# Kernel optimization log

Hardware: AMD Instinct MI355X
Metric: run time of the kernel (lower is better)

## Reference

```python
import jax, jax.numpy as jnp
import numpy as np

B, T, D_MODEL = 2, 2048, 1024
H, D_HEAD, R = 16, 64, 16
CAUSAL = True


def setup_inputs() -> dict:
    key = jax.random.key(0)
    ks = jax.random.split(key, 6)
    return {
        "x": jax.random.normal(ks[0], (B, T, D_MODEL), dtype=jnp.float32),
        "W_qkv": jax.random.normal(ks[1], (D_MODEL, 3 * D_MODEL), dtype=jnp.float32) * 0.02,
        "W_q_lsr": jax.random.normal(ks[2], (H, D_HEAD, R), dtype=jnp.float32) * 0.1,
        "W_k_lsr": jax.random.normal(ks[3], (H, D_HEAD, R), dtype=jnp.float32) * 0.1,
        "core": jax.random.normal(ks[4], (H, R), dtype=jnp.float32),
        "W_o": jax.random.normal(ks[5], (D_MODEL, D_MODEL), dtype=jnp.float32) * 0.02,
    }


def reference(x, W_qkv, W_q_lsr, W_k_lsr, core, W_o):
    Bx, Tx, D = x.shape
    Hh, Dh, Rr = W_q_lsr.shape
    # Fused QKV projection, then split heads -> (B, H, T, D_head)
    qkv = x @ W_qkv  # (B, T, 3D)
    q, k, v = jnp.split(qkv, 3, axis=-1)
    q = q.reshape(Bx, Tx, Hh, Dh).transpose(0, 2, 1, 3)
    k = k.reshape(Bx, Tx, Hh, Dh).transpose(0, 2, 1, 3)
    v = v.reshape(Bx, Tx, Hh, Dh).transpose(0, 2, 1, 3)
    # Low-rank (LSR) projections of q and k; core + 1/sqrt(R) scaling on q side
    scale = 1.0 / jnp.sqrt(jnp.asarray(max(Rr, 1), dtype=jnp.float32))
    q_lr = jnp.einsum('bhtd,hdr->bhtr', q, W_q_lsr) * core[None, :, None, :] * scale
    k_lr = jnp.einsum('bhtd,hdr->bhtr', k, W_k_lsr)
    # Low-rank scores (B, H, T, T)
    scores = jnp.einsum('bhir,bhjr->bhij', q_lr, k_lr)
    if CAUSAL:
        mask = jnp.tril(jnp.ones((Tx, Tx), dtype=bool))
        scores = jnp.where(mask[None, None], scores, -jnp.inf)
    attn = jax.nn.softmax(scores, axis=-1)
    out = jnp.einsum('bhij,bhjd->bhid', attn, v)  # (B, H, T, D_head)
    out = out.transpose(0, 2, 1, 3).reshape(Bx, Tx, D)
    return out @ W_o
```

## Files before the change

kernel.cpp:

```cpp
#include <hip/hip_runtime.h>
#include <hip/hip_bf16.h>

#define BB 2
#define TT 2048
#define DD 1024
#define HH 16
#define DH 64
#define RR 16
#define BT (BB*TT)
#define BH (BB*HH)
#define D3 (3*DD)
#define NC 1536

typedef __bf16 bf16x8 __attribute__((ext_vector_type(8)));
typedef __bf16 bf16x4 __attribute__((ext_vector_type(4)));
typedef float f32x4 __attribute__((ext_vector_type(4)));
typedef short short4v __attribute__((ext_vector_type(4)));

__device__ __forceinline__ float bf2f(unsigned short u) {
  unsigned int v = ((unsigned int)u) << 16;
  return __builtin_bit_cast(float, v);
}
__device__ __forceinline__ unsigned short f2bf(float f) {
  unsigned int x = __builtin_bit_cast(unsigned int, f);
  unsigned int r = x + 0x7fffu + ((x >> 16) & 1u);
  return (unsigned short)(r >> 16);
}
__device__ __forceinline__ short4v pack_bf16x4(float a, float b, float c, float d) {
  uint2 u;
  u.x = (unsigned)f2bf(a) | ((unsigned)f2bf(b) << 16);
  u.y = (unsigned)f2bf(c) | ((unsigned)f2bf(d) << 16);
  return __builtin_bit_cast(short4v, u);
}
__device__ __forceinline__ short4v pack4_cvt(float a, float b, float c, float d) {
  bf16x4 v = {(__bf16)a, (__bf16)b, (__bf16)c, (__bf16)d};
  return __builtin_bit_cast(short4v, v);
}

#define NEG_BIG (-1e30f)

__device__ __forceinline__ void async_copy16(const void* g, void* l) {
  __builtin_amdgcn_global_load_lds((const __attribute__((address_space(1))) void*)g,
                                   (__attribute__((address_space(3))) void*)l, 16, 0, 0);
}

__global__ __launch_bounds__(256) void prep_fused(const float* __restrict__ x,
                                                  const float* __restrict__ Wqkv,
                                                  const float* __restrict__ Wql,
                                                  const float* __restrict__ Wkl,
                                                  const float* __restrict__ core,
                                                  const float* __restrict__ Wo,
                                                  unsigned short* __restrict__ x_bf,
                                                  unsigned short* __restrict__ Wcomb_t,
                                                  unsigned short* __restrict__ Wo_t) {
  __shared__ float tile[32][33];
  __shared__ float Aq[64][65], Ak[64][65], Lq[64][16], Lk[64][16], cs[16];
  const int bid = blockIdx.x, tid = threadIdx.x;
  if (bid < 2048) {
    int i = (bid * 256 + tid) * 8;
    float4 a = *(const float4*)&x[i];
    float4 b = *(const float4*)&x[i + 4];
    unsigned short t[8] = {f2bf(a.x), f2bf(a.y), f2bf(a.z), f2bf(a.w),
                           f2bf(b.x), f2bf(b.y), f2bf(b.z), f2bf(b.w)};
    *(uint4*)&x_bf[i] = *(const uint4*)t;
  } else if (bid < 4096) {
    const float* in; unsigned short* out; int C, coff, lb;
    if (bid < 3072) { in = Wo;   out = Wo_t;    C = DD; coff = 0;    lb = bid - 2048; }
    else            { in = Wqkv; out = Wcomb_t; C = D3; coff = 2048; lb = bid - 3072; }
    const int tx = tid & 31, ty = tid >> 5;
    const int bx = lb & 31, by = lb >> 5;
    const int xx = bx * 32 + tx, y0 = by * 32;
#pragma unroll
    for (int i = 0; i < 32; i += 8)
      tile[ty + i][tx] = in[(size_t)(y0 + ty + i) * C + coff + xx];
    __syncthreads();
    const int xo = y0 + tx, yo0 = bx * 32;
#pragma unroll
    for (int i = 0; i < 32; i += 8)
      out[(size_t)(yo0 + ty + i) * DD + xo] = f2bf(tile[tx][ty + i]);
  } else {
    const int l = bid - 4096;
    const int d0 = (l & 15) * 64, h = l >> 4;
#pragma unroll
    for (int p = 0; p < 16; p++) {
      int idx = p * 256 + tid, dd = idx >> 6, e = idx & 63;
      Aq[dd][e] = Wqkv[(size_t)(d0 + dd) * D3 + h * 64 + e];
      Ak[dd][e] = Wqkv[(size_t)(d0 + dd) * D3 + DD + h * 64 + e];
    }
#pragma unroll
    for (int p = 0; p < 4; p++) {
      int idx = p * 256 + tid, e = idx >> 4, r = idx & 15;
      Lq[e][r] = Wql[h * 1024 + e * 16 + r];
      Lk[e][r] = Wkl[h * 1024 + e * 16 + r];
    }
    if (tid < 16) cs[tid] = core[h * 16 + tid];
    __syncthreads();
    const int dd = tid & 63, rg = tid >> 6;
    float aq[4] = {}, ak[4] = {};
    for (int e = 0; e < 64; e++) {
      float xq = Aq[dd][e], xk = Ak[dd][e];
#pragma unroll
      for (int j = 0; j < 4; j++) {
        aq[j] += xq * Lq[e][rg * 4 + j];
        ak[j] += xk * Lk[e][rg * 4 + j];
      }
    }
#pragma unroll
    for (int j = 0; j < 4; j++) {
      int r = rg * 4 + j;
      Wcomb_t[(size_t)(1024 + h * 16 + r) * DD + d0 + dd] =
          f2bf(aq[j] * cs[r] * (0.25f * 1.4426950408889634f));
      Wcomb_t[(size_t)(1280 + h * 16 + r) * DD + d0 + dd] = f2bf(ak[j]);
    }
  }
}

__device__ __forceinline__ void gemm64_core(const unsigned short* __restrict__ A,
                                            const unsigned short* __restrict__ Bt,
                                            int K, int bm, int bn,
                                            int tid, int g, int c, int wm, int wn,
                                            f32x4 acc[2][4]) {
  __shared__ __attribute__((aligned(16))) unsigned short As[2][64 * 32];
  __shared__ __attribute__((aligned(16))) unsigned short Bs[2][128 * 32];
  const int e0 = tid * 8;
  const int r0 = e0 >> 5, q0 = e0 & 31;
  const unsigned short* Arow = &A[(size_t)(bm * 64 + r0) * K + q0];
  const unsigned short* Brow0 = &Bt[(size_t)(bn * 128 + r0) * K + q0];
  const unsigned short* Brow1 = &Bt[(size_t)(bn * 128 + 64 + r0) * K + q0];
  async_copy16(Arow, &As[0][e0]);
  async_copy16(Brow0, &Bs[0][e0]);
  async_copy16(Brow1, &Bs[0][2048 + e0]);
  __syncthreads();
  const int nsteps = K >> 5;
#pragma unroll 2
  for (int t = 0; t < nsteps; t++) {
    const int cur = t & 1, nxt = cur ^ 1;
    if (t + 1 < nsteps) {
      const int k1 = (t + 1) << 5;
      async_copy16(Arow + k1, &As[nxt][e0]);
      async_copy16(Brow0 + k1, &Bs[nxt][e0]);
      async_copy16(Brow1 + k1, &Bs[nxt][2048 + e0]);
    }
    bf16x8 af[2];
#pragma unroll
    for (int mt = 0; mt < 2; mt++)
      af[mt] = *(const bf16x8*)&As[cur][(wm * 32 + mt * 16 + c) * 32 + g * 8];
#pragma unroll
    for (int nt = 0; nt < 4; nt++) {
      bf16x8 bf = *(const bf16x8*)&Bs[cur][(wn * 64 + nt * 16 + c) * 32 + g * 8];
#pragma unroll
      for (int mt = 0; mt < 2; mt++)
        acc[mt][nt] = __builtin_amdgcn_mfma_f32_16x16x32_bf16(af[mt], bf, acc[mt][nt], 0, 0, 0);
    }
    __syncthreads();
  }
}

__global__ __launch_bounds__(256) void gemm64_f32(const unsigned short* __restrict__ A,
                                                  const unsigned short* __restrict__ Bt,
                                                  float* __restrict__ C,
                                                  int M, int N, int K) {
  const int tid = threadIdx.x, lane = tid & 63;
  const int g = lane >> 4, c = lane & 15;
  const int wid = tid >> 6, wm = wid >> 1, wn = wid & 1;
  const int bm = blockIdx.y, bn = blockIdx.x;
  f32x4 acc[2][4] = {};
  gemm64_core(A, Bt, K, bm, bn, tid, g, c, wm, wn, acc);
#pragma unroll
  for (int mt = 0; mt < 2; mt++)
#pragma unroll
    for (int nt = 0; nt < 4; nt++)
#pragma unroll
      for (int r = 0; r < 4; r++) {
        int row = bm * 64 + wm * 32 + mt * 16 + g * 4 + r;
        int col = bn * 128 + wn * 64 + nt * 16 + c;
        C[(size_t)row * N + col] = acc[mt][nt][r];
      }
}

__global__ __launch_bounds__(256) void gemm_fused(const unsigned short* __restrict__ A,
                                                  const unsigned short* __restrict__ Bt,
                                                  unsigned short* __restrict__ qls,
                                                  unsigned short* __restrict__ klr,
                                                  unsigned short* __restrict__ vt,
                                                  int M, int N, int K) {
  const int tid = threadIdx.x, lane = tid & 63;
  const int g = lane >> 4, c = lane & 15;
  const int wid = tid >> 6, wm = wid >> 1, wn = wid & 1;
  const int bm = blockIdx.y, bn = blockIdx.x;
  f32x4 acc[2][4] = {};
  gemm64_core(A, Bt, K, bm, bn, tid, g, c, wm, wn, acc);
#pragma unroll
  for (int mt = 0; mt < 2; mt++)
#pragma unroll
    for (int nt = 0; nt < 4; nt++) {
      int colb = bn * 128 + wn * 64 + nt * 16;
      int tg0 = bm * 64 + wm * 32 + mt * 16 + g * 4;
      int b = tg0 >> 11, t0 = tg0 & 2047;
      if (colb < 1024) {
        int h = colb >> 6, d = (colb & 63) + c;
        uint2 pk = __builtin_bit_cast(uint2, pack_bf16x4(acc[mt][nt][0], acc[mt][nt][1],
                                                         acc[mt][nt][2], acc[mt][nt][3]));
        size_t idx = (size_t)(b * 16 + h) * (TT / 4) * 256 + (size_t)(t0 >> 2) * 256 + d * 4;
        *(uint2*)&vt[idx] = pk;
      } else if (colb < 1280) {
        int h = (colb - 1024) >> 4;
        size_t base = (size_t)(b * 16 + h) * TT;
#pragma unroll
        for (int r = 0; r < 4; r++)
          qls[(base + t0 + r) * 16 + c] = f2bf(acc[mt][nt][r]);
      } else {
        int h = (colb - 1280) >> 4;
        size_t base = (size_t)(b * 16 + h) * TT;
#pragma unroll
        for (int r = 0; r < 4; r++)
          klr[(base + t0 + r) * 16 + c] = f2bf(acc[mt][nt][r]);
      }
    }
}

__global__ __launch_bounds__(256, 3) void flash_lsr(const unsigned short* __restrict__ qls,
                                                    const unsigned short* __restrict__ klr,
                                                    const unsigned short* __restrict__ vt,
                                                    unsigned short* __restrict__ attn) {
  const int bh = blockIdx.x & 31, b = bh >> 4, h = bh & 15;
  const int qt = 31 - (blockIdx.x >> 5);
  const int tid = threadIdx.x, lane = tid & 63, w = tid >> 6;
  const int g = lane >> 4, c = lane & 15;
  const int q0 = qt * 64, jmax = qt >> 1;

  __shared__ __attribute__((aligned(16))) unsigned short Ks[2][128 * 20];
  __shared__ __attribute__((aligned(16))) unsigned short Vs[2][32 * 264];

  const size_t qbase = (size_t)bh * TT;
  const short4v qf = __builtin_bit_cast(short4v,
      *(const uint2*)&qls[(qbase + q0 + w * 16 + c) * 16 + g * 4]);
  const int qg = q0 + w * 16 + c;
  float mi = NEG_BIG, li = 0.f;
  f32x4 oa[4] = {};
  const f32x4 zero = {0.f, 0.f, 0.f, 0.f};
  const size_t kb = (size_t)bh * TT * 16;
  const size_t vb = (size_t)bh * TT * 64;

  uint4 kr = *(const uint4*)&klr[kb + tid * 8];
  uint4 vr[4];
#pragma unroll
  for (int p = 0; p < 4; p++)
    vr[p] = *(const uint4*)&vt[vb + (p * 256 + tid) * 8];

  int p = 0;
  f32x4 s[8];
  for (int jt = 0; jt <= jmax; jt++) {
    *(uint4*)&Ks[p][(tid >> 1) * 20 + (tid & 1) * 8] = kr;
#pragma unroll
    for (int q = 0; q < 4; q++) {
      int e = (q * 256 + tid) * 8;
      *(uint4*)&Vs[p][(e >> 8) * 264 + (e & 255)] = vr[q];
    }
    __syncthreads();
    if (jt < jmax) {
      kr = *(const uint4*)&klr[kb + (size_t)(jt + 1) * 2048 + tid * 8];
      const unsigned short* vp = &vt[vb + (size_t)(jt + 1) * 8192];
#pragma unroll
      for (int q = 0; q < 4; q++)
        vr[q] = *(const uint4*)&vp[(q * 256 + tid) * 8];
    }
    const unsigned short* Kb = Ks[p];
#pragma unroll
    for (int nt = 0; nt < 8; nt++) {
      short4v kf = __builtin_bit_cast(short4v, *(const uint2*)&Kb[(nt * 16 + c) * 20 + g * 4]);
      s[nt] = __builtin_amdgcn_mfma_f32_16x16x16bf16_1k(kf, qf, zero, 0, 0, 0);
    }
    if (jt == jmax) {
#pragma unroll
      for (int nt = 0; nt < 8; nt++)
#pragma unroll
        for (int r = 0; r < 4; r++) {
          int jg = jt * 128 + nt * 16 + g * 4 + r;
          if (jg > qg) s[nt][r] = NEG_BIG;
        }
    }
    f32x4 vm = s[0];
#pragma unroll
    for (int nt = 1; nt < 8; nt++)
#pragma unroll
      for (int r = 0; r < 4; r++) vm[r] = fmaxf(vm[r], s[nt][r]);
    float rm = fmaxf(fmaxf(vm[0], vm[1]), fmaxf(vm[2], vm[3]));
    rm = fmaxf(rm, __shfl_xor(rm, 16, 64));
    rm = fmaxf(rm, __shfl_xor(rm, 32, 64));
    float mnew = fmaxf(mi, rm);
    float alpha = __builtin_amdgcn_exp2f(mi - mnew);
    mi = mnew;
    f32x4 vs = zero;
#pragma unroll
    for (int nt = 0; nt < 8; nt++)
#pragma unroll
      for (int r = 0; r < 4; r++) {
        float pv = __builtin_amdgcn_exp2f(s[nt][r] - mnew);
        s[nt][r] = pv;
        vs[r] += pv;
      }
    float rs = (vs[0] + vs[1]) + (vs[2] + vs[3]);
    rs += __shfl_xor(rs, 16, 64);
    rs += __shfl_xor(rs, 32, 64);
    li = li * alpha + rs;
#pragma unroll
    for (int nd = 0; nd < 4; nd++)
#pragma unroll
      for (int r = 0; r < 4; r++) oa[nd][r] *= alpha;
    const unsigned short* Vb = Vs[p];
#pragma unroll
    for (int kc = 0; kc < 8; kc++) {
      short4v pf = pack4_cvt(s[kc][0], s[kc][1], s[kc][2], s[kc][3]);
#pragma unroll
      for (int nd = 0; nd < 4; nd++) {
        uint2 vv = *(const uint2*)&Vb[(kc * 4 + g) * 264 + (nd * 16 + c) * 4];
        short4v vf = __builtin_bit_cast(short4v, vv);
        oa[nd] = __builtin_amdgcn_mfma_f32_16x16x16bf16_1k(vf, pf, oa[nd], 0, 0, 0);
      }
    }
    p ^= 1;
  }

  const float inv = 1.f / li;
  const size_t rowb = ((size_t)b * TT + q0 + w * 16 + c) * DD + h * 64;
#pragma unroll
  for (int nd = 0; nd < 4; nd++) {
    short4v pk = pack4_cvt(oa[nd][0] * inv, oa[nd][1] * inv,
                           oa[nd][2] * inv, oa[nd][3] * inv);
    *(uint2*)&attn[rowb + nd * 16 + g * 4] = __builtin_bit_cast(uint2, pk);
  }
}

extern "C" void kernel_launch(void* const* d_in, const int* in_sizes, int n_in,
                              void* d_out, int out_size, void* d_ws, size_t ws_size,
                              hipStream_t stream) {
  const float* x      = (const float*)d_in[0];
  const float* W_qkv  = (const float*)d_in[1];
  const float* W_qlsr = (const float*)d_in[2];
  const float* W_klsr = (const float*)d_in[3];
  const float* core   = (const float*)d_in[4];
  const float* W_o    = (const float*)d_in[5];
  float* out = (float*)d_out;

  char* ws = (char*)d_ws;
  unsigned short* x_bf    = (unsigned short*)ws; ws += (size_t)BT * DD * 2;
  unsigned short* Wcomb_t = (unsigned short*)ws; ws += (size_t)NC * DD * 2;
  unsigned short* Wo_t    = (unsigned short*)ws; ws += (size_t)DD * DD * 2;
  unsigned short* qls     = (unsigned short*)ws; ws += (size_t)BH * TT * 16 * 2;
  unsigned short* klr     = (unsigned short*)ws; ws += (size_t)BH * TT * 16 * 2;
  unsigned short* vt      = (unsigned short*)ws; ws += (size_t)BH * TT * 64 * 2;
  unsigned short* attn    = (unsigned short*)ws; ws += (size_t)BT * DD * 2;

  prep_fused<<<4352, 256, 0, stream>>>(x, W_qkv, W_qlsr, W_klsr, core, W_o,
                                       x_bf, Wcomb_t, Wo_t);
  gemm_fused<<<dim3(NC / 128, BT / 64), 256, 0, stream>>>(x_bf, Wcomb_t, qls, klr, vt, BT, NC, DD);
  flash_lsr<<<dim3(32 * BH), 256, 0, stream>>>(qls, klr, vt, attn);
  gemm64_f32<<<dim3(DD / 128, BT / 64), 256, 0, stream>>>(attn, Wo_t, out, BT, DD, DD);
}
```

Before: 185.9 us.

## Double GEMM K-step to 64 and read V directly from global in flash kernel

The GEMM core now stages 64-wide K slices (two 32-wide halves) per pipeline step, which halves the number of barriers and loop iterations at the cost of doubled LDS use. The flash attention kernel drops the LDS staging of V and has each wave load V fragments straight from global memory (relying on L1/L2) inside the PV MFMA loop. This removes the V LDS writes and shrinks shared memory, which could raise occupancy. The risk is exposed global-load latency on the critical MFMA path, because the V prefetch into registers is gone.

```diff
diff --git a/kernel.cpp b/kernel.cpp
--- a/kernel.cpp
+++ b/kernel.cpp
@@ -120,37 +120,45 @@
                                             int K, int bm, int bn,
                                             int tid, int g, int c, int wm, int wn,
                                             f32x4 acc[2][4]) {
-  __shared__ __attribute__((aligned(16))) unsigned short As[2][64 * 32];
-  __shared__ __attribute__((aligned(16))) unsigned short Bs[2][128 * 32];
+  __shared__ __attribute__((aligned(16))) unsigned short As[2][2 * 2048];
+  __shared__ __attribute__((aligned(16))) unsigned short Bs[2][2 * 4096];
   const int e0 = tid * 8;
   const int r0 = e0 >> 5, q0 = e0 & 31;
-  const unsigned short* Arow = &A[(size_t)(bm * 64 + r0) * K + q0];
-  const unsigned short* Brow0 = &Bt[(size_t)(bn * 128 + r0) * K + q0];
-  const unsigned short* Brow1 = &Bt[(size_t)(bn * 128 + 64 + r0) * K + q0];
-  async_copy16(Arow, &As[0][e0]);
-  async_copy16(Brow0, &Bs[0][e0]);
-  async_copy16(Brow1, &Bs[0][2048 + e0]);
+  const unsigned short* Ar  = &A[(size_t)(bm * 64 + r0) * K + q0];
+  const unsigned short* Br0 = &Bt[(size_t)(bn * 128 + r0) * K + q0];
+  const unsigned short* Br1 = &Bt[(size_t)(bn * 128 + 64 + r0) * K + q0];
+  async_copy16(Ar,       &As[0][e0]);
+  async_copy16(Ar  + 32, &As[0][2048 + e0]);
+  async_copy16(Br0,      &Bs[0][e0]);
+  async_copy16(Br1,      &Bs[0][2048 + e0]);
+  async_copy16(Br0 + 32, &Bs[0][4096 + e0]);
+  async_copy16(Br1 + 32, &Bs[0][4096 + 2048 + e0]);
   __syncthreads();
-  const int nsteps = K >> 5;
-#pragma unroll 2
+  const int nsteps = K >> 6;
   for (int t = 0; t < nsteps; t++) {
     const int cur = t & 1, nxt = cur ^ 1;
     if (t + 1 < nsteps) {
-      const int k1 = (t + 1) << 5;
-      async_copy16(Arow + k1, &As[nxt][e0]);
-      async_copy16(Brow0 + k1, &Bs[nxt][e0]);
-      async_copy16(Brow1 + k1, &Bs[nxt][2048 + e0]);
-    }
-    bf16x8 af[2];
-#pragma unroll
-    for (int mt = 0; mt < 2; mt++)
-      af[mt] = *(const bf16x8*)&As[cur][(wm * 32 + mt * 16 + c) * 32 + g * 8];
-#pragma unroll
-    for (int nt = 0; nt < 4; nt++) {
-      bf16x8 bf = *(const bf16x8*)&Bs[cur][(wn * 64 + nt * 16 + c) * 32 + g * 8];
+      const int k1 = (t + 1) << 6;
+      async_copy16(Ar  + k1,      &As[nxt][e0]);
+      async_copy16(Ar  + k1 + 32, &As[nxt][2048 + e0]);
+      async_copy16(Br0 + k1,      &Bs[nxt][e0]);
+      async_copy16(Br1 + k1,      &Bs[nxt][2048 + e0]);
+      async_copy16(Br0 + k1 + 32, &Bs[nxt][4096 + e0]);
+      async_copy16(Br1 + k1 + 32, &Bs[nxt][4096 + 2048 + e0]);
+    }
+#pragma unroll
+    for (int p = 0; p < 2; p++) {
+      bf16x8 af[2];
 #pragma unroll
       for (int mt = 0; mt < 2; mt++)
-        acc[mt][nt] = __builtin_amdgcn_mfma_f32_16x16x32_bf16(af[mt], bf, acc[mt][nt], 0, 0, 0);
+        af[mt] = *(const bf16x8*)&As[cur][p * 2048 + (wm * 32 + mt * 16 + c) * 32 + g * 8];
+#pragma unroll
+      for (int nt = 0; nt < 4; nt++) {
+        bf16x8 bf = *(const bf16x8*)&Bs[cur][p * 4096 + (wn * 64 + nt * 16 + c) * 32 + g * 8];
+#pragma unroll
+        for (int mt = 0; mt < 2; mt++)
+          acc[mt][nt] = __builtin_amdgcn_mfma_f32_16x16x32_bf16(af[mt], bf, acc[mt][nt], 0, 0, 0);
+      }
     }
     __syncthreads();
   }
@@ -230,7 +238,6 @@
   const int q0 = qt * 64, jmax = qt >> 1;
 
   __shared__ __attribute__((aligned(16))) unsigned short Ks[2][128 * 20];
-  __shared__ __attribute__((aligned(16))) unsigned short Vs[2][32 * 264];
 
   const size_t qbase = (size_t)bh * TT;
   const short4v qf = __builtin_bit_cast(short4v,
@@ -243,28 +250,14 @@
   const size_t vb = (size_t)bh * TT * 64;
 
   uint4 kr = *(const uint4*)&klr[kb + tid * 8];
-  uint4 vr[4];
-#pragma unroll
-  for (int p = 0; p < 4; p++)
-    vr[p] = *(const uint4*)&vt[vb + (p * 256 + tid) * 8];
 
   int p = 0;
   f32x4 s[8];
   for (int jt = 0; jt <= jmax; jt++) {
     *(uint4*)&Ks[p][(tid >> 1) * 20 + (tid & 1) * 8] = kr;
-#pragma unroll
-    for (int q = 0; q < 4; q++) {
-      int e = (q * 256 + tid) * 8;
-      *(uint4*)&Vs[p][(e >> 8) * 264 + (e & 255)] = vr[q];
-    }
     __syncthreads();
-    if (jt < jmax) {
+    if (jt < jmax)
       kr = *(const uint4*)&klr[kb + (size_t)(jt + 1) * 2048 + tid * 8];
-      const unsigned short* vp = &vt[vb + (size_t)(jt + 1) * 8192];
-#pragma unroll
-      for (int q = 0; q < 4; q++)
-        vr[q] = *(const uint4*)&vp[(q * 256 + tid) * 8];
-    }
     const unsigned short* Kb = Ks[p];
 #pragma unroll
     for (int nt = 0; nt < 8; nt++) {
@@ -308,13 +301,13 @@
     for (int nd = 0; nd < 4; nd++)
 #pragma unroll
       for (int r = 0; r < 4; r++) oa[nd][r] *= alpha;
-    const unsigned short* Vb = Vs[p];
+    const unsigned short* vp = &vt[vb + (size_t)jt * 8192];
 #pragma unroll
     for (int kc = 0; kc < 8; kc++) {
       short4v pf = pack4_cvt(s[kc][0], s[kc][1], s[kc][2], s[kc][3]);
 #pragma unroll
       for (int nd = 0; nd < 4; nd++) {
-        uint2 vv = *(const uint2*)&Vb[(kc * 4 + g) * 264 + (nd * 16 + c) * 4];
+        uint2 vv = *(const uint2*)&vp[(kc * 4 + g) * 256 + (nd * 16 + c) * 4];
         short4v vf = __builtin_bit_cast(short4v, vv);
         oa[nd] = __builtin_amdgcn_mfma_f32_16x16x16bf16_1k(vf, pf, oa[nd], 0, 0, 0);
       }
```

Measured after the change: 174.6 us. 6.1% less time.
